# Kernel optimization log

Hardware: AMD Instinct MI355X
Metric: run time of the kernel (lower is better)

The kernel has to match this reference:

```python
import jax, jax.numpy as jnp
import numpy as np

B, N, IN_F, OUT_F, H = 4, 2048, 128, 128, 4
D = OUT_F // H  # head_dim = 32
NEG_SLOPE = 0.2


def setup_inputs() -> dict:
    key = jax.random.key(0)
    k1, k2, k3, k4, k5 = jax.random.split(key, 5)
    x = jax.random.normal(k1, (B, N, IN_F), dtype=jnp.float32)
    adj = jax.random.randint(k2, (N, N), 0, 2, dtype=jnp.int32)
    adj = adj.at[jnp.arange(N), jnp.arange(N)].set(1)  # self-loops
    # xavier-uniform-like init
    lim_w = float(np.sqrt(6.0 / (IN_F + OUT_F)))
    W = jax.random.uniform(k3, (OUT_F, IN_F), minval=-lim_w, maxval=lim_w, dtype=jnp.float32)
    lim_a = float(np.sqrt(6.0 / (H + D)))
    a_src = jax.random.uniform(k4, (H, D), minval=-lim_a, maxval=lim_a, dtype=jnp.float32)
    a_dst = jax.random.uniform(k5, (H, D), minval=-lim_a, maxval=lim_a, dtype=jnp.float32)
    return {"x": x, "adj": adj, "W": W, "a_src": a_src, "a_dst": a_dst}


def reference(x, adj, W, a_src, a_dst):
    Bx, Nx, _ = x.shape
    # linear projection: (B,N,out) -> (B,N,H,D)
    h = jnp.einsum('bni,oi->bno', x, W).reshape(Bx, Nx, H, D)
    e_src = jnp.einsum('bnhd,hd->bnh', h, a_src)  # (B,N,H)
    e_dst = jnp.einsum('bnhd,hd->bnh', h, a_dst)  # (B,N,H)
    # scores: (B,N_src,H,N_dst)
    scores = jax.nn.leaky_relu(
        e_src[:, :, :, None] + e_dst.transpose(0, 2, 1)[:, None, :, :],
        negative_slope=NEG_SLOPE,
    )
    mask = adj[None, :, None, :]  # (1,N,1,N)
    scores = jnp.where(mask == 0, -jnp.inf, scores)
    attn = jax.nn.softmax(scores, axis=-1)  # (B,N,H,N); dropout is identity at eval
    out = jnp.einsum('bnhm,bmhd->bnhd', attn, h)  # (B,N,H,D)
    return out.reshape(Bx, Nx, H * D)
```

## Files before the change

kernel.cpp:

```cpp
#include <hip/hip_runtime.h>
#include <math.h>

#define BB 4
#define NN 2048
#define FF 128
#define HH 4
#define DD 32
#define NEG_SLOPE 0.2f
#define LOG2E 1.4426950408889634f

typedef __attribute__((ext_vector_type(8))) short short8;
typedef __attribute__((ext_vector_type(4))) float floatx4;
typedef __attribute__((ext_vector_type(2))) float floatx2;

__device__ __forceinline__ float exp2_fast(float x) {
#if __has_builtin(__builtin_amdgcn_exp2f)
    return __builtin_amdgcn_exp2f(x);
#else
    return exp2f(x);
#endif
}

__device__ __forceinline__ int bit_mask(unsigned int w, int bit) {
#if __has_builtin(__builtin_amdgcn_sbfe)
    return __builtin_amdgcn_sbfe((int)w, bit, 1);
#else
    return ((int)(w << (31 - bit))) >> 31;
#endif
}

__device__ __forceinline__ unsigned int pack2_rtne(float lo, float hi) {
    unsigned int ul = __float_as_uint(lo); ul += 0x7FFFu + ((ul >> 16) & 1u);
    unsigned int uh = __float_as_uint(hi); uh += 0x7FFFu + ((uh >> 16) & 1u);
    return (ul >> 16) | (uh & 0xFFFF0000u);
}

__global__ __launch_bounds__(256) void k_prep(const float* __restrict__ x,
                                              const float* __restrict__ W,
                                              const float* __restrict__ a_src,
                                              const float* __restrict__ a_dst,
                                              const int* __restrict__ adj,
                                              unsigned short* __restrict__ ht,
                                              float* __restrict__ es_t,
                                              float* __restrict__ ed_t,
                                              unsigned int* __restrict__ bits) {
    __shared__ unsigned short wbf[128][144];
    __shared__ unsigned short hbf[128][24];
    __shared__ float vs_s[HH][FF], vd_s[HH][FF];
    __shared__ float as_s[FF], ad_s[FF];
    int t = threadIdx.x;

    if (blockIdx.x >= 512) {
        int idx = (blockIdx.x - 512) * 256 + t;
        int n = idx >> 6, w = idx & 63;
        const int4* base = (const int4*)(adj + (size_t)n * NN + w * 32);
        unsigned int word = 0;
#pragma unroll
        for (int q = 0; q < 8; ++q) {
            int4 a = base[q];
            word |= ((unsigned int)(a.x & 1)) << (q * 4 + 0);
            word |= ((unsigned int)(a.y & 1)) << (q * 4 + 1);
            word |= ((unsigned int)(a.z & 1)) << (q * 4 + 2);
            word |= ((unsigned int)(a.w & 1)) << (q * 4 + 3);
        }
        bits[idx] = word;
        return;
    }

    int m0g = blockIdx.x * 16;
    int b = m0g >> 11;
    int m_block = m0g & 2047;

    if (t < FF) { as_s[t] = a_src[t]; ad_s[t] = a_dst[t]; }
#pragma unroll
    for (int k = 0; k < 8; ++k) {
        int idx = t + k * 256;
        int row = idx >> 4, ch = idx & 15;
        const float* wp = W + (size_t)row * FF + ch * 8;
        float4 v0 = *(const float4*)wp;
        float4 v1 = *(const float4*)(wp + 4);
        unsigned int u[4];
        u[0] = pack2_rtne(v0.x, v0.y); u[1] = pack2_rtne(v0.z, v0.w);
        u[2] = pack2_rtne(v1.x, v1.y); u[3] = pack2_rtne(v1.z, v1.w);
        *(int4*)&wbf[row][ch * 8] = *(const int4*)u;
    }
    __syncthreads();

    {
        int i = t & 127;
        float acc4[4] = {0.f, 0.f, 0.f, 0.f};
        if (t < 128) {
            for (int o = 0; o < 128; ++o) {
                float wv = __uint_as_float(((unsigned int)wbf[o][i]) << 16);
                acc4[o >> 5] += wv * as_s[o];
            }
#pragma unroll
            for (int hd = 0; hd < 4; ++hd) vs_s[hd][i] = acc4[hd];
        } else {
            for (int o = 0; o < 128; ++o) {
                float wv = __uint_as_float(((unsigned int)wbf[o][i]) << 16);
                acc4[o >> 5] += wv * ad_s[o];
            }
#pragma unroll
            for (int hd = 0; hd < 4; ++hd) vd_s[hd][i] = acc4[hd];
        }
    }

    int wid = t >> 6, lane = t & 63;
    int r = lane & 15, q = lane >> 4;
    floatx4 acc[2] = {{0.f,0.f,0.f,0.f},{0.f,0.f,0.f,0.f}};
    const float* xrow = x + (size_t)(m0g + r) * FF + q * 8;
#pragma unroll
    for (int kk = 0; kk < 4; ++kk) {
        float4 a0 = *(const float4*)(xrow + kk * 32);
        float4 a1 = *(const float4*)(xrow + kk * 32 + 4);
        union { short8 s8; unsigned int u[4]; } af;
        af.u[0] = pack2_rtne(a0.x, a0.y); af.u[1] = pack2_rtne(a0.z, a0.w);
        af.u[2] = pack2_rtne(a1.x, a1.y); af.u[3] = pack2_rtne(a1.z, a1.w);
#pragma unroll
        for (int c = 0; c < 2; ++c) {
            int o = (wid * 2 + c) * 16 + r;
            short8 bf = *(const short8*)&wbf[o][kk * 32 + q * 8];
            acc[c] = __builtin_amdgcn_mfma_f32_16x16x32_bf16(af.s8, bf, acc[c], 0, 0, 0);
        }
    }
#pragma unroll
    for (int c = 0; c < 2; ++c) {
        int o = (wid * 2 + c) * 16 + r;
        unsigned int u2[2];
        u2[0] = pack2_rtne(acc[c][0], acc[c][1]);
        u2[1] = pack2_rtne(acc[c][2], acc[c][3]);
        *(int2*)&hbf[o][q * 4] = *(const int2*)u2;
    }
    __syncthreads();

    if (t < 128) {
        int hd = t >> 5, d = t & 31;
        unsigned short* op = ht + ((size_t)(b * HH + hd) * DD + d) * NN + m_block;
        *(int4*)op       = *(const int4*)&hbf[t][0];
        *(int4*)(op + 8) = *(const int4*)&hbf[t][8];
    }
    {
        int m = t >> 4, sg = t & 15;
        const float* xp = x + (size_t)(m0g + m) * FF + sg * 8;
        float4 x0 = *(const float4*)xp;
        float4 x1 = *(const float4*)(xp + 4);
#pragma unroll
        for (int hd = 0; hd < 4; ++hd) {
            const float* vsp = &vs_s[hd][sg * 8];
            const float* vdp = &vd_s[hd][sg * 8];
            float es = x0.x * vsp[0] + x0.y * vsp[1] + x0.z * vsp[2] + x0.w * vsp[3]
                     + x1.x * vsp[4] + x1.y * vsp[5] + x1.z * vsp[6] + x1.w * vsp[7];
            float ed = x0.x * vdp[0] + x0.y * vdp[1] + x0.z * vdp[2] + x0.w * vdp[3]
                     + x1.x * vdp[4] + x1.y * vdp[5] + x1.z * vdp[6] + x1.w * vdp[7];
#pragma unroll
            for (int k = 1; k < 16; k <<= 1) {
                es += __shfl_xor(es, k);
                ed += __shfl_xor(ed, k);
            }
            if (sg == 0) {
                size_t eb = (size_t)(b * HH + hd) * NN + m_block + m;
                es_t[eb] = es * LOG2E;
                float ee = ed * LOG2E;
                float2 pr;
                pr.x = exp2_fast(ee);
                pr.y = exp2_fast(NEG_SLOPE * ee);
                *(float2*)(ed_t + eb * 2) = pr;
            }
        }
    }
}

#define HBW 528
#define HOF 264
__global__ __launch_bounds__(512) void k_attn(
        const unsigned short* __restrict__ ht,
        const unsigned int* __restrict__ bits,
        const float* __restrict__ es_t,
        const float* __restrict__ ed_t,
        float* __restrict__ out) {
    __shared__ unsigned short hb[DD * HBW];
    __shared__ float ep[NN * 2];
    int t = threadIdx.x;
    int n0 = blockIdx.x * 64;
    int bh = blockIdx.y;
    int b = bh >> 2, head = bh & 3;

    int wid = t >> 6, lane = t & 63;
    int q = lane >> 4, r = lane & 15;
    int qo = q * 8;
    int half = wid >> 2, wsub = wid & 3;
    int n_l = wsub * 16 + r;

    const unsigned short* htp = ht + (size_t)bh * DD * NN;

    {
        const float4* src = (const float4*)(ed_t + (size_t)bh * NN * 2);
        ((float4*)ep)[t]       = src[t];
        ((float4*)ep)[t + 512] = src[t + 512];
    }
#pragma unroll
    for (int k2 = 0; k2 < 4; ++k2) {
        int j = t + k2 * 512;
        int hf = j >> 10, jj = j & 1023;
        int d = jj >> 5, c16 = jj & 31;
        int4 v = *(const int4*)(htp + (size_t)d * NN + hf * 1024 + c16 * 8);
        *(int4*)&hb[d * HBW + hf * HOF + c16 * 8] = v;
    }
    float esv = es_t[(size_t)bh * NN + n0 + n_l];
    float tn = exp2_fast(-0.8f * esv);
    __syncthreads();

    floatx4 acc0 = {0.f, 0.f, 0.f, 0.f};
    floatx4 acc1 = {0.f, 0.f, 0.f, 0.f};
    floatx4 accd = {0.f, 0.f, 0.f, 0.f};
    union { short8 s8; int i[4]; } ones;
    ones.i[0] = 0x3F803F80; ones.i[1] = 0x3F803F80;
    ones.i[2] = 0x3F803F80; ones.i[3] = 0x3F803F80;

    const unsigned short* hrow0 = &hb[r * HBW + half * HOF + qo];
    const unsigned short* hrow1 = &hb[(r + 16) * HBW + half * HOF + qo];
    const unsigned int* bpb = bits + (size_t)(n0 + n_l) * 64 + half * 32;

    for (int ck = 0; ck < 4; ++ck) {
        int4 bw0 = *(const int4*)(bpb + ck * 8);
        int4 bw1 = *(const int4*)(bpb + ck * 8 + 4);
        const float* pb_ck = ep + (half * 1024 + ck * 256) * 2;
#pragma unroll
        for (int g = 0; g < 2; ++g) {
            int4 bwv = g ? bw1 : bw0;
#pragma unroll
            for (int c = 0; c < 4; ++c) {
                unsigned int word = (unsigned int)((&bwv.x)[c]);
                int mb = g * 128 + c * 32;
                unsigned int wq = word >> qo;
                const float* pbase = pb_ck + (mb + qo) * 2;
                union { short8 s8; int i[4]; } af;
#pragma unroll
                for (int jp = 0; jp < 4; ++jp) {
                    float4 d2 = *(const float4*)(pbase + jp * 4);
                    float w0 = fmaxf(d2.x, tn * d2.y);
                    float w1 = fmaxf(d2.z, tn * d2.w);
                    int m0 = bit_mask(wq, 2 * jp);
                    int m1 = bit_mask(wq, 2 * jp + 1);
                    w0 = __uint_as_float(__float_as_uint(w0) & (unsigned int)m0);
                    w1 = __uint_as_float(__float_as_uint(w1) & (unsigned int)m1);
                    af.i[jp] = __builtin_amdgcn_perm(__float_as_uint(w1),
                                                     __float_as_uint(w0),
                                                     0x07060302u);
                }
                short8 b0 = *(const short8*)(hrow0 + mb);
                short8 b1 = *(const short8*)(hrow1 + mb);
                acc0 = __builtin_amdgcn_mfma_f32_16x16x32_bf16(af.s8, b0, acc0, 0, 0, 0);
                acc1 = __builtin_amdgcn_mfma_f32_16x16x32_bf16(af.s8, b1, acc1, 0, 0, 0);
                accd = __builtin_amdgcn_mfma_f32_16x16x32_bf16(af.s8, ones.s8, accd, 0, 0, 0);
            }
        }
        __syncthreads();
        if (ck < 3) {
            int ckn = ck + 1;
#pragma unroll
            for (int k2 = 0; k2 < 4; ++k2) {
                int j = t + k2 * 512;
                int hf = j >> 10, jj = j & 1023;
                int d = jj >> 5, c16 = jj & 31;
                int4 v = *(const int4*)(htp + (size_t)d * NN + hf * 1024
                                        + ckn * 256 + c16 * 8);
                *(int4*)&hb[d * HBW + hf * HOF + c16 * 8] = v;
            }
        }
        __syncthreads();
    }

    float* scr = (float*)hb;
    if (half == 1) {
        int base = (wsub * 64 + lane) * 12;
        *(floatx4*)&scr[base + 0] = acc0;
        *(floatx4*)&scr[base + 4] = acc1;
        *(floatx4*)&scr[base + 8] = accd;
    }
    __syncthreads();
    if (half == 0) {
        int base = (wsub * 64 + lane) * 12;
        floatx4 p0 = *(const floatx4*)&scr[base + 0];
        floatx4 p1 = *(const floatx4*)&scr[base + 4];
        floatx4 pd = *(const floatx4*)&scr[base + 8];
#pragma unroll
        for (int k = 0; k < 4; ++k) {
            acc0[k] += p0[k]; acc1[k] += p1[k]; accd[k] += pd[k];
        }
#pragma unroll
        for (int reg = 0; reg < 4; ++reg) {
            int nrow = n0 + wsub * 16 + q * 4 + reg;
            float inv = 1.0f / accd[reg];
            float* op = out + ((size_t)(b * NN + nrow)) * FF + head * DD;
            op[r]      = acc0[reg] * inv;
            op[16 + r] = acc1[reg] * inv;
        }
    }
}

extern "C" void kernel_launch(void* const* d_in, const int* in_sizes, int n_in,
                              void* d_out, int out_size, void* d_ws, size_t ws_size,
                              hipStream_t stream) {
    const float* x     = (const float*)d_in[0];
    const int*   adj   = (const int*)d_in[1];
    const float* W     = (const float*)d_in[2];
    const float* a_src = (const float*)d_in[3];
    const float* a_dst = (const float*)d_in[4];
    float* out = (float*)d_out;

    float* es_t = (float*)d_ws;
    float* ed_t = es_t + (size_t)BB * HH * NN;
    unsigned int* bits = (unsigned int*)(ed_t + (size_t)BB * HH * NN * 2);
    unsigned short* ht = (unsigned short*)(bits + (size_t)NN * (NN / 32));

    hipLaunchKernelGGL(k_prep, dim3(1024), dim3(256), 0, stream,
                       x, W, a_src, a_dst, adj, ht, es_t, ed_t, bits);
    hipLaunchKernelGGL(k_attn, dim3(NN / 64, BB * HH), dim3(512), 0, stream,
                       ht, bits, es_t, ed_t, out);
}
```

Before: 98.27 us.

## Halve query rows per block and split key range four ways across warps

Each attention block now handles 32 destination rows instead of 64. Its eight warps are arranged as four key-quarters by two row groups rather than two halves by four row groups, and partial accumulators are reduced across the four quarters through shared memory. The grid doubles to put more blocks across the CUs, and launch bounds request 6 waves per SIMD. The cost is that each block reloads the full h tile and ep array for half as many rows, which doubles per-row global and LDS staging traffic, and the final reduction grows.

```diff
diff --git a/kernel.cpp b/kernel.cpp
--- a/kernel.cpp
+++ b/kernel.cpp
@@ -171,9 +171,9 @@
     }
 }
 
-#define HBW 528
-#define HOF 264
-__global__ __launch_bounds__(512) void k_attn(
+#define HBW 548
+#define QOF 136
+__global__ __launch_bounds__(512, 6) void k_attn(
         const unsigned short* __restrict__ ht,
         const unsigned int* __restrict__ bits,
         const float* __restrict__ es_t,
@@ -182,15 +182,15 @@
     __shared__ unsigned short hb[DD * HBW];
     __shared__ float ep[NN * 2];
     int t = threadIdx.x;
-    int n0 = blockIdx.x * 64;
+    int n0 = blockIdx.x * 32;
     int bh = blockIdx.y;
     int b = bh >> 2, head = bh & 3;
 
     int wid = t >> 6, lane = t & 63;
     int q = lane >> 4, r = lane & 15;
     int qo = q * 8;
-    int half = wid >> 2, wsub = wid & 3;
-    int n_l = wsub * 16 + r;
+    int qt = wid >> 1, ng = wid & 1;
+    int n_l = ng * 16 + r;
 
     const unsigned short* htp = ht + (size_t)bh * DD * NN;
 
@@ -202,10 +202,10 @@
 #pragma unroll
     for (int k2 = 0; k2 < 4; ++k2) {
         int j = t + k2 * 512;
-        int hf = j >> 10, jj = j & 1023;
-        int d = jj >> 5, c16 = jj & 31;
-        int4 v = *(const int4*)(htp + (size_t)d * NN + hf * 1024 + c16 * 8);
-        *(int4*)&hb[d * HBW + hf * HOF + c16 * 8] = v;
+        int qq = j >> 9, jj = j & 511;
+        int d = jj >> 4, c16 = jj & 15;
+        int4 v = *(const int4*)(htp + (size_t)d * NN + qq * 512 + c16 * 8);
+        *(int4*)&hb[d * HBW + qq * QOF + c16 * 8] = v;
     }
     float esv = es_t[(size_t)bh * NN + n0 + n_l];
     float tn = exp2_fast(-0.8f * esv);
@@ -218,43 +218,38 @@
     ones.i[0] = 0x3F803F80; ones.i[1] = 0x3F803F80;
     ones.i[2] = 0x3F803F80; ones.i[3] = 0x3F803F80;
 
-    const unsigned short* hrow0 = &hb[r * HBW + half * HOF + qo];
-    const unsigned short* hrow1 = &hb[(r + 16) * HBW + half * HOF + qo];
-    const unsigned int* bpb = bits + (size_t)(n0 + n_l) * 64 + half * 32;
+    const unsigned short* hrow0 = &hb[r * HBW + qt * QOF + qo];
+    const unsigned short* hrow1 = &hb[(r + 16) * HBW + qt * QOF + qo];
+    const unsigned int* bpb = bits + (size_t)(n0 + n_l) * 64 + qt * 16;
 
     for (int ck = 0; ck < 4; ++ck) {
-        int4 bw0 = *(const int4*)(bpb + ck * 8);
-        int4 bw1 = *(const int4*)(bpb + ck * 8 + 4);
-        const float* pb_ck = ep + (half * 1024 + ck * 256) * 2;
-#pragma unroll
-        for (int g = 0; g < 2; ++g) {
-            int4 bwv = g ? bw1 : bw0;
-#pragma unroll
-            for (int c = 0; c < 4; ++c) {
-                unsigned int word = (unsigned int)((&bwv.x)[c]);
-                int mb = g * 128 + c * 32;
-                unsigned int wq = word >> qo;
-                const float* pbase = pb_ck + (mb + qo) * 2;
-                union { short8 s8; int i[4]; } af;
-#pragma unroll
-                for (int jp = 0; jp < 4; ++jp) {
-                    float4 d2 = *(const float4*)(pbase + jp * 4);
-                    float w0 = fmaxf(d2.x, tn * d2.y);
-                    float w1 = fmaxf(d2.z, tn * d2.w);
-                    int m0 = bit_mask(wq, 2 * jp);
-                    int m1 = bit_mask(wq, 2 * jp + 1);
-                    w0 = __uint_as_float(__float_as_uint(w0) & (unsigned int)m0);
-                    w1 = __uint_as_float(__float_as_uint(w1) & (unsigned int)m1);
-                    af.i[jp] = __builtin_amdgcn_perm(__float_as_uint(w1),
-                                                     __float_as_uint(w0),
-                                                     0x07060302u);
-                }
-                short8 b0 = *(const short8*)(hrow0 + mb);
-                short8 b1 = *(const short8*)(hrow1 + mb);
-                acc0 = __builtin_amdgcn_mfma_f32_16x16x32_bf16(af.s8, b0, acc0, 0, 0, 0);
-                acc1 = __builtin_amdgcn_mfma_f32_16x16x32_bf16(af.s8, b1, acc1, 0, 0, 0);
-                accd = __builtin_amdgcn_mfma_f32_16x16x32_bf16(af.s8, ones.s8, accd, 0, 0, 0);
-            }
+        int4 bwv = *(const int4*)(bpb + ck * 4);
+        const float* pb_ck = ep + (qt * 512 + ck * 128) * 2;
+#pragma unroll
+        for (int c = 0; c < 4; ++c) {
+            unsigned int word = (unsigned int)((&bwv.x)[c]);
+            int mb = c * 32;
+            unsigned int wq = word >> qo;
+            const float* pbase = pb_ck + (mb + qo) * 2;
+            union { short8 s8; int i[4]; } af;
+#pragma unroll
+            for (int jp = 0; jp < 4; ++jp) {
+                float4 d2 = *(const float4*)(pbase + jp * 4);
+                float w0 = fmaxf(d2.x, tn * d2.y);
+                float w1 = fmaxf(d2.z, tn * d2.w);
+                int m0 = bit_mask(wq, 2 * jp);
+                int m1 = bit_mask(wq, 2 * jp + 1);
+                w0 = __uint_as_float(__float_as_uint(w0) & (unsigned int)m0);
+                w1 = __uint_as_float(__float_as_uint(w1) & (unsigned int)m1);
+                af.i[jp] = __builtin_amdgcn_perm(__float_as_uint(w1),
+                                                 __float_as_uint(w0),
+                                                 0x07060302u);
+            }
+            short8 b0 = *(const short8*)(hrow0 + mb);
+            short8 b1 = *(const short8*)(hrow1 + mb);
+            acc0 = __builtin_amdgcn_mfma_f32_16x16x32_bf16(af.s8, b0, acc0, 0, 0, 0);
+            acc1 = __builtin_amdgcn_mfma_f32_16x16x32_bf16(af.s8, b1, acc1, 0, 0, 0);
+            accd = __builtin_amdgcn_mfma_f32_16x16x32_bf16(af.s8, ones.s8, accd, 0, 0, 0);
         }
         __syncthreads();
         if (ck < 3) {
@@ -262,36 +257,39 @@
 #pragma unroll
             for (int k2 = 0; k2 < 4; ++k2) {
                 int j = t + k2 * 512;
-                int hf = j >> 10, jj = j & 1023;
-                int d = jj >> 5, c16 = jj & 31;
-                int4 v = *(const int4*)(htp + (size_t)d * NN + hf * 1024
-                                        + ckn * 256 + c16 * 8);
-                *(int4*)&hb[d * HBW + hf * HOF + c16 * 8] = v;
+                int qq = j >> 9, jj = j & 511;
+                int d = jj >> 4, c16 = jj & 15;
+                int4 v = *(const int4*)(htp + (size_t)d * NN + qq * 512
+                                        + ckn * 128 + c16 * 8);
+                *(int4*)&hb[d * HBW + qq * QOF + c16 * 8] = v;
             }
         }
         __syncthreads();
     }
 
     float* scr = (float*)hb;
-    if (half == 1) {
-        int base = (wsub * 64 + lane) * 12;
+    if (qt != 0) {
+        int base = (((qt - 1) * 2 + ng) * 64 + lane) * 12;
         *(floatx4*)&scr[base + 0] = acc0;
         *(floatx4*)&scr[base + 4] = acc1;
         *(floatx4*)&scr[base + 8] = accd;
     }
     __syncthreads();
-    if (half == 0) {
-        int base = (wsub * 64 + lane) * 12;
-        floatx4 p0 = *(const floatx4*)&scr[base + 0];
-        floatx4 p1 = *(const floatx4*)&scr[base + 4];
-        floatx4 pd = *(const floatx4*)&scr[base + 8];
-#pragma unroll
-        for (int k = 0; k < 4; ++k) {
-            acc0[k] += p0[k]; acc1[k] += p1[k]; accd[k] += pd[k];
+    if (qt == 0) {
+#pragma unroll
+        for (int p = 0; p < 3; ++p) {
+            int base = ((p * 2 + ng) * 64 + lane) * 12;
+            floatx4 p0 = *(const floatx4*)&scr[base + 0];
+            floatx4 p1 = *(const floatx4*)&scr[base + 4];
+            floatx4 pd = *(const floatx4*)&scr[base + 8];
+#pragma unroll
+            for (int k = 0; k < 4; ++k) {
+                acc0[k] += p0[k]; acc1[k] += p1[k]; accd[k] += pd[k];
+            }
         }
 #pragma unroll
         for (int reg = 0; reg < 4; ++reg) {
-            int nrow = n0 + wsub * 16 + q * 4 + reg;
+            int nrow = n0 + ng * 16 + q * 4 + reg;
             float inv = 1.0f / accd[reg];
             float* op = out + ((size_t)(b * NN + nrow)) * FF + head * DD;
             op[r]      = acc0[reg] * inv;
@@ -317,6 +315,6 @@
 
     hipLaunchKernelGGL(k_prep, dim3(1024), dim3(256), 0, stream,
                        x, W, a_src, a_dst, adj, ht, es_t, ed_t, bits);
-    hipLaunchKernelGGL(k_attn, dim3(NN / 64, BB * HH), dim3(512), 0, stream,
+    hipLaunchKernelGGL(k_attn, dim3(NN / 32, BB * HH), dim3(512), 0, stream,
                        ht, bits, es_t, ed_t, out);
 }
```

After: 123.2 us. 1.25x slower.
